# Kernel tuning notes

Hardware: AMD Instinct MI355X
Metric: run time of the kernel (lower is better)

Reference implementation:

```python
import jax, jax.numpy as jnp
import numpy as np

B, S, IN, HID, H, D, FF = 8, 2048, 512, 512, 8, 64, 2048
EPS = 1e-5


def layer_norm(x, g, b):
    m = jnp.mean(x, axis=-1, keepdims=True)
    v = jnp.mean(jnp.square(x - m), axis=-1, keepdims=True)
    return (x - m) * jax.lax.rsqrt(v + EPS) * g + b


def delta_rule(q, k, v, beta):
    # q,k,v: [S,B,H,D]; beta: [S,B,H,1]
    # W_t = W_{t-1} + beta_t*(v_t - W_{t-1} k_t) k_t^T ; out_t = W_t q_t
    def step(W, inp):
        qt, kt, vt, bt = inp
        wk = jnp.einsum('bhde,bhe->bhd', W, kt)
        v_new = bt * (vt - wk)
        W = W + jnp.einsum('bhd,bhe->bhde', v_new, kt)
        out = jnp.einsum('bhde,bhe->bhd', W, qt)
        return W, out

    bsz = q.shape[1]
    W0 = jnp.zeros((bsz, H, D, D), dtype=q.dtype)
    _, outs = jax.lax.scan(step, W0, (q, k, v, beta))
    return outs  # [S,B,H,D]


def fast_ff(x, ln_g, ln_b, slow_w, out_w):
    # x: [S,B,HID]
    slen, bsz, _ = x.shape
    h = layer_norm(x, ln_g, ln_b)
    qkvb = jnp.einsum('sbi,oi->sbo', h, slow_w).reshape(slen, bsz, H, 3 * D + 1)
    q, k, v, beta = jnp.split(qkvb, [D, 2 * D, 3 * D], axis=-1)
    q = jax.nn.softmax(q, axis=-1)
    k = jax.nn.softmax(k, axis=-1)
    beta = jax.nn.sigmoid(beta)
    attn = delta_rule(q, k, v, beta)  # [S,B,H,D]
    o = jnp.einsum('sbd,od->sbo', attn.reshape(slen, bsz, H * D), out_w)
    return x + o


def ffn(x, ln_g, ln_b, w1, b1, w2, b2):
    h = layer_norm(x, ln_g, ln_b)
    h = jax.nn.relu(jnp.einsum('sbi,fi->sbf', h, w1) + b1)
    return x + jnp.einsum('sbf,of->sbo', h, w2) + b2


def setup_inputs() -> dict:
    key = jax.random.key(0)
    ks = jax.random.split(key, 8)
    s = 0.02
    return {
        'x': jax.random.normal(ks[0], (B, S, IN), jnp.float32),
        'ip_w': s * jax.random.normal(ks[1], (HID, IN), jnp.float32),
        'ip_b': jnp.zeros((HID,), jnp.float32),
        'fw_ln_g': jnp.ones((2, HID), jnp.float32),
        'fw_ln_b': jnp.zeros((2, HID), jnp.float32),
        'fw_slow_w': s * jax.random.normal(ks[2], (2, H * (3 * D + 1), HID), jnp.float32),
        'fw_out_w': s * jax.random.normal(ks[3], (2, HID, H * D), jnp.float32),
        'ff_ln_g': jnp.ones((HID,), jnp.float32),
        'ff_ln_b': jnp.zeros((HID,), jnp.float32),
        'ff_w1': s * jax.random.normal(ks[4], (FF, HID), jnp.float32),
        'ff_b1': jnp.zeros((FF,), jnp.float32),
        'ff_w2': s * jax.random.normal(ks[5], (HID, FF), jnp.float32),
        'ff_b2': jnp.zeros((HID,), jnp.float32),
    }


def reference(x, ip_w, ip_b, fw_ln_g, fw_ln_b, fw_slow_w, fw_out_w,
              ff_ln_g, ff_ln_b, ff_w1, ff_b1, ff_w2, ff_b2):
    out = jnp.einsum('bsi,hi->bsh', x, ip_w) + ip_b  # input_proj
    out = out.transpose(1, 0, 2)  # [S,B,HID]
    out = fast_ff(out, fw_ln_g[0], fw_ln_b[0], fw_slow_w[0], fw_out_w[0])
    out = ffn(out, ff_ln_g, ff_ln_b, ff_w1, ff_b1, ff_w2, ff_b2)
    out = fast_ff(out, fw_ln_g[1], fw_ln_b[1], fw_slow_w[1], fw_out_w[1])
    return out.transpose(1, 0, 2)  # [B,S,HID]
```

## Files before the change

### kernel.cpp

```cpp
#include <hip/hip_runtime.h>
#include <hip/hip_bf16.h>

#define B_    8
#define S_    2048
#define HID_  512
#define H_    8
#define D_    64
#define FF_   2048
#define QN_   1664
#define NCH_  32
#define SLOWSTRIDE (1544 * 512)

typedef unsigned short u16;
typedef __attribute__((ext_vector_type(8))) short short8;
typedef __attribute__((ext_vector_type(4))) float f32x4;

__device__ __forceinline__ u16 f2bf(float x) {
  unsigned u = __builtin_bit_cast(unsigned, x);
  unsigned r = (u + 0x7FFFu + ((u >> 16) & 1u)) >> 16;
  return (u16)r;
}
__device__ __forceinline__ float bf2f(u16 v) {
  return __builtin_bit_cast(float, (unsigned)v << 16);
}
__device__ __forceinline__ void gload16(const void* g, void* l) {
  __builtin_amdgcn_global_load_lds(
      (const __attribute__((address_space(1))) unsigned int*)g,
      (__attribute__((address_space(3))) unsigned int*)l, 16, 0, 0);
}

template<int FS, int GS>
__device__ __forceinline__ void prod64(const u16* __restrict__ F,
                                       const u16* __restrict__ G,
                                       int wrow0, int lane, f32x4 acc[4])
{
  short8 f0 = *(const short8*)&F[(wrow0 + (lane & 15)) * FS + ((lane >> 4) * 8)];
  short8 f1 = *(const short8*)&F[(wrow0 + (lane & 15)) * FS + 32 + ((lane >> 4) * 8)];
  #pragma unroll
  for (int c0 = 0; c0 < 4; ++c0) {
    short8 g0 = *(const short8*)&G[(c0 * 16 + (lane & 15)) * GS + ((lane >> 4) * 8)];
    short8 g1 = *(const short8*)&G[(c0 * 16 + (lane & 15)) * GS + 32 + ((lane >> 4) * 8)];
    acc[c0] = __builtin_amdgcn_mfma_f32_16x16x32_bf16(f0, g0, acc[c0], 0, 0, 0);
    acc[c0] = __builtin_amdgcn_mfma_f32_16x16x32_bf16(f1, g1, acc[c0], 0, 0, 0);
  }
}

template<bool BIAS, bool RELU, bool RES, bool OUTBF, bool TRANS, bool QKVB>
__global__ __launch_bounds__(256, 4) void gemm_bf(
    const u16* __restrict__ A, const u16* __restrict__ W,
    const float* __restrict__ bias, const float* __restrict__ res,
    void* __restrict__ Cout, int M, int N, int K, int nx)
{
  __shared__ __align__(16) u16 SH[16384];
  const int tid = threadIdx.x, lane = tid & 63, wv = tid >> 6;
  const int nwg = gridDim.x;
  const int l = ((blockIdx.x & 7) * (nwg >> 3)) + (blockIdx.x >> 3);
  const int bm = (l / nx) * 128, bn = (l % nx) * 128;
  const int wr = wv >> 1, wc = wv & 1;
  const int row16 = lane & 15, kg = lane >> 4;
  const int srow = lane >> 2;
  const int ssoff = ((lane & 3) ^ (srow & 3)) * 16;

  f32x4 acc[4][4] = {};
  const int ktiles = K >> 5;

  auto STAGE = [&](int buf, int kt) {
    u16* As = &SH[buf * 8192];
    u16* Bs = &SH[buf * 8192 + 4096];
    #pragma unroll
    for (int i = 0; i < 2; ++i) {
      const int r = i * 64 + wv * 16;
      const char* ga = (const char*)(A + (size_t)(bm + r + srow) * K + (size_t)kt * 32) + ssoff;
      gload16(ga, &As[r * 32]);
      const char* gw = (const char*)(W + (size_t)(bn + r + srow) * K + (size_t)kt * 32) + ssoff;
      gload16(gw, &Bs[r * 32]);
    }
  };

  STAGE(0, 0);
  __syncthreads();
  int buf = 0;
  for (int kt = 0; kt < ktiles; ++kt) {
    if (kt + 1 < ktiles) STAGE(buf ^ 1, kt + 1);
    const u16* As = &SH[buf * 8192];
    const u16* Bs = &SH[buf * 8192 + 4096];
    short8 af[4], bf_[4];
    #pragma unroll
    for (int m = 0; m < 4; ++m) {
      const int lrow = wr * 64 + m * 16 + row16;
      af[m] = *(const short8*)&As[lrow * 32 + (kg ^ (lrow & 3)) * 8];
    }
    #pragma unroll
    for (int n = 0; n < 4; ++n) {
      const int lrow = wc * 64 + n * 16 + row16;
      bf_[n] = *(const short8*)&Bs[lrow * 32 + (kg ^ (lrow & 3)) * 8];
    }
    #pragma unroll
    for (int m = 0; m < 4; ++m)
      #pragma unroll
      for (int n = 0; n < 4; ++n)
        acc[m][n] = __builtin_amdgcn_mfma_f32_16x16x32_bf16(af[m], bf_[n], acc[m][n], 0, 0, 0);
    __syncthreads();
    buf ^= 1;
  }

  if (QKVB) {
    const int span0 = bn + wc * 64;
    #pragma unroll
    for (int m = 0; m < 4; ++m) {
      #pragma unroll
      for (int j = 0; j < 4; ++j) {
        if (span0 < 1024) {
          float v0 = acc[m][0][j], v1 = acc[m][1][j];
          float v2 = acc[m][2][j], v3 = acc[m][3][j];
          float mx = fmaxf(fmaxf(v0, v1), fmaxf(v2, v3));
          #pragma unroll
          for (int off = 1; off < 16; off <<= 1) mx = fmaxf(mx, __shfl_xor(mx, off));
          float e0 = __expf(v0 - mx), e1 = __expf(v1 - mx);
          float e2 = __expf(v2 - mx), e3 = __expf(v3 - mx);
          float s = (e0 + e1) + (e2 + e3);
          #pragma unroll
          for (int off = 1; off < 16; off <<= 1) s += __shfl_xor(s, off);
          float r = 1.f / s;
          acc[m][0][j] = e0 * r; acc[m][1][j] = e1 * r;
          acc[m][2][j] = e2 * r; acc[m][3][j] = e3 * r;
        } else if (span0 >= 1536) {
          #pragma unroll
          for (int n = 0; n < 4; ++n)
            acc[m][n][j] = 1.f / (1.f + __expf(-acc[m][n][j]));
        }
      }
    }
  }

  float* LD = (float*)SH;
  #pragma unroll
  for (int p = 0; p < 4; ++p) {
    if (p) __syncthreads();
    if (wr == (p >> 1)) {
      #pragma unroll
      for (int mm = 0; mm < 2; ++mm) {
        const int m = (p & 1) * 2 + mm;
        #pragma unroll
        for (int n = 0; n < 4; ++n)
          #pragma unroll
          for (int j = 0; j < 4; ++j)
            LD[(mm * 16 + kg * 4 + j) * 132 + wc * 64 + n * 16 + row16] = acc[m][n][j];
      }
    }
    __syncthreads();
    #pragma unroll
    for (int step = 0; step < 4; ++step) {
      int linear = step * 256 + tid;
      int row = linear >> 5, q = linear & 31;
      float4 v = *(const float4*)&LD[row * 132 + q * 4];
      const int grow = bm + p * 32 + row;
      const int gcol = bn + q * 4;
      if (BIAS) {
        float4 b4 = *(const float4*)&bias[gcol];
        v.x += b4.x; v.y += b4.y; v.z += b4.z; v.w += b4.w;
      }
      if (RES) {
        float4 r4 = *(const float4*)&res[(size_t)grow * N + gcol];
        v.x += r4.x; v.y += r4.y; v.z += r4.z; v.w += r4.w;
      }
      if (RELU) {
        v.x = fmaxf(v.x, 0.f); v.y = fmaxf(v.y, 0.f);
        v.z = fmaxf(v.z, 0.f); v.w = fmaxf(v.w, 0.f);
      }
      size_t gr = TRANS ? ((size_t)(grow & 7) * S_ + (grow >> 3)) : (size_t)grow;
      if (OUTBF) {
        uint2 pk;
        pk.x = (unsigned)f2bf(v.x) | ((unsigned)f2bf(v.y) << 16);
        pk.y = (unsigned)f2bf(v.z) | ((unsigned)f2bf(v.w) << 16);
        *(uint2*)&((u16*)Cout)[gr * N + gcol] = pk;
      } else {
        *(float4*)&((float*)Cout)[gr * N + gcol] = v;
      }
    }
  }
}

__global__ __launch_bounds__(256) void conv_w(const float* __restrict__ s,
                                              u16* __restrict__ d, int n, int npad)
{
  int i = blockIdx.x * 256 + threadIdx.x;
  if (i < npad) d[i] = (i < n) ? f2bf(s[i]) : (u16)0;
}

__global__ __launch_bounds__(256) void conv_slow(const float* __restrict__ s,
                                                 u16* __restrict__ d)
{
  int r = blockIdx.x;
  int src;
  if (r < 512)       src = (r >> 6) * 193 + (r & 63);
  else if (r < 1024) src = ((r - 512) >> 6) * 193 + 64 + (r & 63);
  else if (r < 1536) src = ((r - 1024) >> 6) * 193 + 128 + (r & 63);
  else if (r < 1544) src = (r - 1536) * 193 + 192;
  else               src = -1;
  for (int c = threadIdx.x; c < 512; c += 256)
    d[(size_t)r * 512 + c] = (src >= 0) ? f2bf(s[(size_t)src * 512 + c]) : (u16)0;
}

__global__ __launch_bounds__(64) void conv_x(const float* __restrict__ x,
                                             u16* __restrict__ xbf)
{
  size_t m = blockIdx.x;
  size_t s = m >> 3, b = m & 7;
  const float4* src = (const float4*)(x + (b * (size_t)S_ + s) * HID_);
  float4 v0 = src[threadIdx.x], v1 = src[64 + threadIdx.x];
  u16* dst = xbf + m * HID_;
  uint2 p0, p1;
  p0.x = (unsigned)f2bf(v0.x) | ((unsigned)f2bf(v0.y) << 16);
  p0.y = (unsigned)f2bf(v0.z) | ((unsigned)f2bf(v0.w) << 16);
  p1.x = (unsigned)f2bf(v1.x) | ((unsigned)f2bf(v1.y) << 16);
  p1.y = (unsigned)f2bf(v1.z) | ((unsigned)f2bf(v1.w) << 16);
  *(uint2*)&dst[threadIdx.x * 4] = p0;
  *(uint2*)&dst[256 + threadIdx.x * 4] = p1;
}

__global__ __launch_bounds__(64) void ln_bf(const float* __restrict__ x,
    const float* __restrict__ g, const float* __restrict__ bt,
    u16* __restrict__ o)
{
  size_t row = blockIdx.x;
  int lane = threadIdx.x;
  const float4* xr = (const float4*)(x + row * HID_);
  float4 v0 = xr[lane];
  float4 v1 = xr[64 + lane];
  float s  = v0.x + v0.y + v0.z + v0.w + v1.x + v1.y + v1.z + v1.w;
  float ss = v0.x*v0.x + v0.y*v0.y + v0.z*v0.z + v0.w*v0.w
           + v1.x*v1.x + v1.y*v1.y + v1.z*v1.z + v1.w*v1.w;
  #pragma unroll
  for (int off = 32; off; off >>= 1) {
    s  += __shfl_xor(s, off);
    ss += __shfl_xor(ss, off);
  }
  float mean = s * (1.f / HID_);
  float inv  = rsqrtf(ss * (1.f / HID_) - mean * mean + 1e-5f);
  const float4* gv = (const float4*)g;
  const float4* bv = (const float4*)bt;
  float4 g0 = gv[lane], g1 = gv[64 + lane];
  float4 b0 = bv[lane], b1 = bv[64 + lane];
  uint2 p0, p1;
  p0.x = (unsigned)f2bf((v0.x - mean) * inv * g0.x + b0.x)
       | ((unsigned)f2bf((v0.y - mean) * inv * g0.y + b0.y) << 16);
  p0.y = (unsigned)f2bf((v0.z - mean) * inv * g0.z + b0.z)
       | ((unsigned)f2bf((v0.w - mean) * inv * g0.w + b0.w) << 16);
  p1.x = (unsigned)f2bf((v1.x - mean) * inv * g1.x + b1.x)
       | ((unsigned)f2bf((v1.y - mean) * inv * g1.y + b1.y) << 16);
  p1.y = (unsigned)f2bf((v1.z - mean) * inv * g1.z + b1.z)
       | ((unsigned)f2bf((v1.w - mean) * inv * g1.w + b1.w) << 16);
  u16* ov = o + row * HID_;
  *(uint2*)&ov[lane * 4] = p0;
  *(uint2*)&ov[256 + lane * 4] = p1;
}

__global__ __launch_bounds__(256, 3) void delta_p1(const u16* __restrict__ qf,
                                                   u16* __restrict__ MTg,
                                                   u16* __restrict__ Ng,
                                                   u16* __restrict__ CKg,
                                                   u16* __restrict__ U0Tg)
{
  __shared__ __align__(16) u16 Kb[64 * 72];
  __shared__ __align__(16) u16 AmKT[64 * 72];
  __shared__ __align__(16) u16 stV[16 * 72];
  __shared__ __align__(16) u16 stK[16 * 72];
  __shared__ __align__(16) u16 CKTb[64 * 72];
  __shared__ __align__(16) u16 U0Tb[64 * 72];
  __shared__ float bet[64];

  const int id5 = blockIdx.x, bh = id5 >> 5;
  const int b = bh & 7, h = bh >> 3, t0 = (id5 & 31) * 64;
  const int tid = threadIdx.x, lane = tid & 63, wv = tid >> 6;
  const int wid = wv, wrow0 = wv * 16;
  const size_t mb = (size_t)id5 * 4096;

  #pragma unroll
  for (int p = 0; p < 2; ++p) {
    int linear = p * 256 + tid, row = linear >> 3, seg = linear & 7;
    uint4 k4 = *(const uint4*)&qf[((size_t)(t0 + row) * B_ + b) * QN_ + 512 + h * 64 + seg * 8];
    *(short8*)&Kb[row * 72 + seg * 8] = __builtin_bit_cast(short8, k4);
  }
  if (tid < 64) bet[tid] = bf2f(qf[((size_t)(t0 + tid) * B_ + b) * QN_ + 1536 + h]);
  __syncthreads();

  {
    f32x4 a[4] = {};
    prod64<72, 72>(Kb, Kb, wrow0, lane, a);
    #pragma unroll
    for (int c0 = 0; c0 < 4; ++c0)
      #pragma unroll
      for (int j = 0; j < 4; ++j) {
        int row = wrow0 + (lane >> 4) * 4 + j, col = c0 * 16 + (lane & 15);
        AmKT[col * 72 + row] = f2bf(bet[row] * a[c0][j]);
      }
  }

  float uv[16], uk[16];
  #pragma unroll
  for (int i = 0; i < 16; ++i) {
    const int row = wrow0 + i;
    const float bt_ = bet[row];
    uv[i] = bt_ * bf2f(qf[((size_t)(t0 + row) * B_ + b) * QN_ + 1024 + h * 64 + lane]);
    uk[i] = bt_ * bf2f(Kb[row * 72 + lane]);
  }
  __syncthreads();

  #pragma unroll 1
  for (int blk = 0; blk < 4; ++blk) {
    if (wid == blk) {
      const int r0 = blk * 16;
      #pragma unroll
      for (int jj = 0; jj < 15; ++jj) {
        short8 a0 = *(const short8*)&AmKT[(r0 + jj) * 72 + r0];
        short8 a1 = *(const short8*)&AmKT[(r0 + jj) * 72 + r0 + 8];
        float uvj = uv[jj], ukj = uk[jj];
        #pragma unroll
        for (int t = jj + 1; t < 16; ++t) {
          float a = bf2f((u16)(t < 8 ? a0[t] : a1[t - 8]));
          uv[t] = fmaf(-a, uvj, uv[t]);
          uk[t] = fmaf(-a, ukj, uk[t]);
        }
      }
      {
        union { u16 u[16]; short8 s[2]; } pv, pk;
        #pragma unroll
        for (int i = 0; i < 16; ++i) { pv.u[i] = f2bf(uv[i]); pk.u[i] = f2bf(uk[i]); }
        *(short8*)&stV[lane * 18 + 0] = pv.s[0];
        *(short8*)&stV[lane * 18 + 8] = pv.s[1];
        *(short8*)&stK[lane * 18 + 0] = pk.s[0];
        *(short8*)&stK[lane * 18 + 8] = pk.s[1];
      }
    }
    __syncthreads();
    if (wid > blk) {
      const int r0 = blk * 16;
      #pragma unroll
      for (int jj = 0; jj < 16; ++jj) {
        short8 a0 = *(const short8*)&AmKT[(r0 + jj) * 72 + wrow0];
        short8 a1 = *(const short8*)&AmKT[(r0 + jj) * 72 + wrow0 + 8];
        float sv = bf2f(stV[lane * 18 + jj]);
        float sk = bf2f(stK[lane * 18 + jj]);
        #pragma unroll
        for (int i = 0; i < 16; ++i) {
          float a = bf2f((u16)(i < 8 ? a0[i] : a1[i - 8]));
          uv[i] = fmaf(-a, sv, uv[i]);
          uk[i] = fmaf(-a, sk, uk[i]);
        }
      }
    }
    __syncthreads();
  }

  {
    union { u16 u[16]; short8 s[2]; } pk, pu;
    #pragma unroll
    for (int i = 0; i < 16; ++i) { pk.u[i] = f2bf(uk[i]); pu.u[i] = f2bf(uv[i]); }
    *(short8*)&CKTb[lane * 72 + wrow0]     = pk.s[0];
    *(short8*)&CKTb[lane * 72 + wrow0 + 8] = pk.s[1];
    *(short8*)&U0Tb[lane * 72 + wrow0]     = pu.s[0];
    *(short8*)&U0Tb[lane * 72 + wrow0 + 8] = pu.s[1];
  }
  const int prow = tid >> 2, pc0 = (tid & 3) * 16;
  {
    union { u16 u[16]; short8 s[2]; } pt;
    #pragma unroll
    for (int i = 0; i < 16; ++i) pt.u[i] = Kb[(pc0 + i) * 72 + prow];
    *(short8*)&AmKT[prow * 72 + pc0]     = pt.s[0];
    *(short8*)&AmKT[prow * 72 + pc0 + 8] = pt.s[1];
  }
  __syncthreads();

  {
    f32x4 am[4] = {}, an[4] = {};
    prod64<72, 72>(AmKT, CKTb, wrow0, lane, am);
    prod64<72, 72>(U0Tb, AmKT, wrow0, lane, an);
    #pragma unroll
    for (int c0 = 0; c0 < 4; ++c0)
      #pragma unroll
      for (int j = 0; j < 4; ++j) {
        int row = wrow0 + (lane >> 4) * 4 + j, col = c0 * 16 + (lane & 15);
        MTg[mb + (size_t)row * 64 + col] = f2bf(am[c0][j]);
        Ng[mb + (size_t)row * 64 + col]  = f2bf(an[c0][j]);
      }
    union { u16 u[16]; uint4 v[2]; } pc;
    #pragma unroll
    for (int i = 0; i < 16; ++i) pc.u[i] = CKTb[(pc0 + i) * 72 + prow];
    *(uint4*)&CKg[mb + prow * 64 + pc0]     = pc.v[0];
    *(uint4*)&CKg[mb + prow * 64 + pc0 + 8] = pc.v[1];
    short8 a0 = *(const short8*)&U0Tb[prow * 72 + pc0];
    short8 a1 = *(const short8*)&U0Tb[prow * 72 + pc0 + 8];
    *(uint4*)&U0Tg[mb + prow * 64 + pc0]     = __builtin_bit_cast(uint4, a0);
    *(uint4*)&U0Tg[mb + prow * 64 + pc0 + 8] = __builtin_bit_cast(uint4, a1);
  }
}

__global__ __launch_bounds__(256, 1) void delta_p2(const u16* __restrict__ MTg,
                                                   const u16* __restrict__ Ng,
                                                   u16* __restrict__ Wsnap)
{
  __shared__ float Ws[64][65];
  __shared__ __align__(16) u16 Wbf[64 * 72];
  __shared__ __align__(16) u16 MTb[64 * 72];
  __shared__ __align__(16) u16 Nb[64 * 72];
  const int bh = blockIdx.x;
  const int tid = threadIdx.x, lane = tid & 63, wv = tid >> 6, wrow0 = wv * 16;
  const int prow = tid >> 2, pc0 = (tid & 3) * 16;

  for (int i = tid; i < 64 * 65; i += 256) (&Ws[0][0])[i] = 0.f;
  for (int i = tid; i < 64 * 72; i += 256) Wbf[i] = 0;
  __syncthreads();

  size_t base = (size_t)bh * NCH_ * 4096;
  uint4 rm0 = *(const uint4*)&MTg[base + prow * 64 + pc0];
  uint4 rm1 = *(const uint4*)&MTg[base + prow * 64 + pc0 + 8];
  uint4 rn0 = *(const uint4*)&Ng[base + prow * 64 + pc0];
  uint4 rn1 = *(const uint4*)&Ng[base + prow * 64 + pc0 + 8];

  for (int j = 0; j < NCH_; ++j) {
    *(short8*)&MTb[prow * 72 + pc0]     = __builtin_bit_cast(short8, rm0);
    *(short8*)&MTb[prow * 72 + pc0 + 8] = __builtin_bit_cast(short8, rm1);
    *(short8*)&Nb[prow * 72 + pc0]      = __builtin_bit_cast(short8, rn0);
    *(short8*)&Nb[prow * 72 + pc0 + 8]  = __builtin_bit_cast(short8, rn1);
    {
      size_t sb = base + (size_t)j * 4096;
      short8 w0 = *(const short8*)&Wbf[prow * 72 + pc0];
      short8 w1 = *(const short8*)&Wbf[prow * 72 + pc0 + 8];
      *(uint4*)&Wsnap[sb + prow * 64 + pc0]     = __builtin_bit_cast(uint4, w0);
      *(uint4*)&Wsnap[sb + prow * 64 + pc0 + 8] = __builtin_bit_cast(uint4, w1);
    }
    if (j + 1 < NCH_) {
      size_t nb2 = base + (size_t)(j + 1) * 4096;
      rm0 = *(const uint4*)&MTg[nb2 + prow * 64 + pc0];
      rm1 = *(const uint4*)&MTg[nb2 + prow * 64 + pc0 + 8];
      rn0 = *(const uint4*)&Ng[nb2 + prow * 64 + pc0];
      rn1 = *(const uint4*)&Ng[nb2 + prow * 64 + pc0 + 8];
    }
    __syncthreads();
    f32x4 a[4] = {};
    prod64<72, 72>(Wbf, MTb, wrow0, lane, a);
    #pragma unroll
    for (int c0 = 0; c0 < 4; ++c0)
      #pragma unroll
      for (int jj = 0; jj < 4; ++jj) {
        int row = wrow0 + (lane >> 4) * 4 + jj, col = c0 * 16 + (lane & 15);
        float w = Ws[row][col] + bf2f(Nb[row * 72 + col]) - a[c0][jj];
        Ws[row][col] = w;
        Wbf[row * 72 + col] = f2bf(w);
      }
    __syncthreads();
  }
}

__global__ __launch_bounds__(256, 2) void delta_p3(const u16* __restrict__ qf,
                                                   const u16* __restrict__ Wsnap,
                                                   const u16* __restrict__ CKg,
                                                   const u16* __restrict__ U0Tg,
                                                   u16* __restrict__ attnb)
{
  __shared__ __align__(16) u16 Qb[64 * 72];
  __shared__ __align__(16) u16 Kb[64 * 72];
  __shared__ __align__(16) u16 W0b[64 * 72];
  __shared__ __align__(16) u16 CKb[64 * 72];
  __shared__ __align__(16) u16 U0Tb[64 * 72];
  __shared__ __align__(16) u16 Gb[64 * 72];
  __shared__ __align__(16) u16 UTb[64 * 72];

  const int id5 = blockIdx.x, bh = id5 >> 5;
  const int b = bh & 7, h = bh >> 3, t0 = (id5 & 31) * 64;
  const int tid = threadIdx.x, lane = tid & 63, wv = tid >> 6, wrow0 = wv * 16;
  const int prow = tid >> 2, pc0 = (tid & 3) * 16;
  const size_t mb = (size_t)id5 * 4096;

  #pragma unroll
  for (int p = 0; p < 2; ++p) {
    int linear = p * 256 + tid, row = linear >> 3, seg = linear & 7;
    size_t gb = ((size_t)(t0 + row) * B_ + b) * QN_;
    uint4 q4 = *(const uint4*)&qf[gb + h * 64 + seg * 8];
    uint4 k4 = *(const uint4*)&qf[gb + 512 + h * 64 + seg * 8];
    uint4 w4 = *(const uint4*)&Wsnap[mb + (size_t)row * 64 + seg * 8];
    *(short8*)&Qb[row * 72 + seg * 8]  = __builtin_bit_cast(short8, q4);
    *(short8*)&Kb[row * 72 + seg * 8]  = __builtin_bit_cast(short8, k4);
    *(short8*)&W0b[row * 72 + seg * 8] = __builtin_bit_cast(short8, w4);
  }
  {
    uint4 c0v = *(const uint4*)&CKg[mb + prow * 64 + pc0];
    uint4 c1v = *(const uint4*)&CKg[mb + prow * 64 + pc0 + 8];
    uint4 u0v = *(const uint4*)&U0Tg[mb + prow * 64 + pc0];
    uint4 u1v = *(const uint4*)&U0Tg[mb + prow * 64 + pc0 + 8];
    *(short8*)&CKb[prow * 72 + pc0]      = __builtin_bit_cast(short8, c0v);
    *(short8*)&CKb[prow * 72 + pc0 + 8]  = __builtin_bit_cast(short8, c1v);
    *(short8*)&U0Tb[prow * 72 + pc0]     = __builtin_bit_cast(short8, u0v);
    *(short8*)&U0Tb[prow * 72 + pc0 + 8] = __builtin_bit_cast(short8, u1v);
  }
  __syncthreads();

  f32x4 ag[4] = {}, ac[4] = {}, ab[4] = {};
  prod64<72, 72>(Qb, Kb, wrow0, lane, ag);
  prod64<72, 72>(W0b, CKb, wrow0, lane, ac);
  prod64<72, 72>(Qb, W0b, wrow0, lane, ab);

  #pragma unroll
  for (int c0 = 0; c0 < 4; ++c0)
    #pragma unroll
    for (int j = 0; j < 4; ++j) {
      int row = wrow0 + (lane >> 4) * 4 + j, col = c0 * 16 + (lane & 15);
      Gb[row * 72 + col]  = f2bf(col <= row ? ag[c0][j] : 0.f);
      UTb[row * 72 + col] = f2bf(bf2f(U0Tb[row * 72 + col]) - ac[c0][j]);
    }
  __syncthreads();

  prod64<72, 72>(Gb, UTb, wrow0, lane, ab);

  #pragma unroll
  for (int c0 = 0; c0 < 4; ++c0)
    #pragma unroll
    for (int j = 0; j < 4; ++j) {
      int row = wrow0 + (lane >> 4) * 4 + j, col = c0 * 16 + (lane & 15);
      attnb[((size_t)(t0 + row) * B_ + b) * HID_ + h * 64 + col] = f2bf(ab[c0][j]);
    }
}

extern "C" void kernel_launch(void* const* d_in, const int* in_sizes, int n_in,
                              void* d_out, int out_size, void* d_ws, size_t ws_size,
                              hipStream_t stream)
{
  const float* x        = (const float*)d_in[0];
  const float* ip_w     = (const float*)d_in[1];
  const float* ip_b     = (const float*)d_in[2];
  const float* fw_ln_g  = (const float*)d_in[3];
  const float* fw_ln_b  = (const float*)d_in[4];
  const float* fw_slow_w = (const float*)d_in[5];
  const float* fw_out_w  = (const float*)d_in[6];
  const float* ff_ln_g  = (const float*)d_in[7];
  const float* ff_ln_b  = (const float*)d_in[8];
  const float* ff_w1    = (const float*)d_in[9];
  const float* ff_b1    = (const float*)d_in[10];
  const float* ff_w2    = (const float*)d_in[11];
  const float* ff_b2    = (const float*)d_in[12];
  float* out = (float*)d_out;

  const int M = B_ * S_;
  const size_t matN = (size_t)64 * NCH_ * 4096;

  const size_t nIp = 512 * 512, nOut = 512 * 512;
  const size_t nSlow = (size_t)QN_ * 512;
  const size_t nW1 = (size_t)FF_ * 512, nW2 = (size_t)512 * FF_;
  const size_t nXbf = (size_t)M * HID_;
  const size_t poolElems = nIp + 2 * nSlow + 2 * nOut + nW1 + nW2 + nXbf + matN;

  size_t need = (size_t)M * HID_ * 4
              + ((size_t)M * QN_ + 2 * matN + poolElems) * 2;
  if (ws_size < need) return;

  float* cur   = (float*)d_ws;
  u16*   qkvbf = (u16*)(cur + (size_t)M * HID_);
  u16*   attnSlot = qkvbf + (size_t)M * QN_;
  u16*   MTg   = attnSlot;
  u16*   Ng    = MTg + matN;
  u16*   attnb = attnSlot;
  u16*   CKg   = (u16*)out;
  u16*   U0Tg  = CKg + matN;
  u16*   tmpbf = (u16*)out;
  u16*   hiddenb = qkvbf;

  u16* pool = attnSlot + 2 * matN;
  u16* ipwb   = pool;               pool += nIp;
  u16* slowb0 = pool;               pool += nSlow;
  u16* slowb1 = pool;               pool += nSlow;
  u16* outwb0 = pool;               pool += nOut;
  u16* outwb1 = pool;               pool += nOut;
  u16* w1b    = pool;               pool += nW1;
  u16* w2b    = pool;               pool += nW2;
  u16* Wsnap  = pool;               pool += matN;
  u16* xbf    = pool;

  dim3 blk(256);

  conv_w<<<(nIp + 255) / 256, blk, 0, stream>>>(ip_w, ipwb, nIp, nIp);
  conv_slow<<<QN_, blk, 0, stream>>>(fw_slow_w, slowb0);
  conv_slow<<<QN_, blk, 0, stream>>>(fw_slow_w + (size_t)SLOWSTRIDE, slowb1);
  conv_w<<<(nOut + 255) / 256, blk, 0, stream>>>(fw_out_w, outwb0, nOut, nOut);
  conv_w<<<(nOut + 255) / 256, blk, 0, stream>>>(fw_out_w + (size_t)512 * 512, outwb1, nOut, nOut);
  conv_w<<<(nW1 + 255) / 256, blk, 0, stream>>>(ff_w1, w1b, nW1, nW1);
  conv_w<<<(nW2 + 255) / 256, blk, 0, stream>>>(ff_w2, w2b, nW2, nW2);
  conv_x<<<M, 64, 0, stream>>>(x, xbf);

  gemm_bf<true, false, false, false, false, false><<<4 * 128, blk, 0, stream>>>(
      xbf, ipwb, ip_b, nullptr, cur, M, HID_, HID_, 4);

  for (int layer = 0; layer < 2; ++layer) {
    u16* slowb = layer ? slowb1 : slowb0;
    u16* outwb = layer ? outwb1 : outwb0;

    ln_bf<<<M, 64, 0, stream>>>(cur, fw_ln_g + layer * HID_, fw_ln_b + layer * HID_, tmpbf);
    gemm_bf<false, false, false, true, false, true><<<13 * 128, blk, 0, stream>>>(
        tmpbf, slowb, nullptr, nullptr, qkvbf, M, QN_, HID_, 13);
    delta_p1<<<64 * NCH_, 256, 0, stream>>>(qkvbf, MTg, Ng, CKg, U0Tg);
    delta_p2<<<64, 256, 0, stream>>>(MTg, Ng, Wsnap);
    delta_p3<<<64 * NCH_, 256, 0, stream>>>(qkvbf, Wsnap, CKg, U0Tg, attnb);
    if (layer == 0) {
      gemm_bf<false, false, true, false, false, false><<<4 * 128, blk, 0, stream>>>(
          attnb, outwb, nullptr, cur, cur, M, HID_, HID_, 4);
      ln_bf<<<M, 64, 0, stream>>>(cur, ff_ln_g, ff_ln_b, tmpbf);
      gemm_bf<true, true, false, true, false, false><<<16 * 128, blk, 0, stream>>>(
          tmpbf, w1b, ff_b1, nullptr, hiddenb, M, FF_, HID_, 16);
      gemm_bf<true, false, true, false, false, false><<<4 * 128, blk, 0, stream>>>(
          hiddenb, w2b, ff_b2, cur, cur, M, HID_, FF_, 4);
    } else {
      gemm_bf<false, false, true, false, true, false><<<4 * 128, blk, 0, stream>>>(
          attnb, outwb, nullptr, cur, out, M, HID_, HID_, 4);
    }
  }
}
```

Baseline: 521.8 us.

## Split delta state recurrence across row groups and fuse weight conversions

The sequential chunk-state kernel is split so each block owns 16 rows of the 64x64 state. This gives 256 blocks instead of 64 and shortens per-step MFMA work, at the cost of each block redundantly loading the full MT chunk. The seven weight-conversion launches are merged into one kernel, cutting launch overhead. The output kernel reuses the Q/K shared buffers for G/UT, which needs an extra barrier, to lower LDS use and allow three blocks per CU.

```diff
diff --git a/kernel.cpp b/kernel.cpp
--- a/kernel.cpp
+++ b/kernel.cpp
@@ -181,25 +181,54 @@
   }
 }
 
-__global__ __launch_bounds__(256) void conv_w(const float* __restrict__ s,
-                                              u16* __restrict__ d, int n, int npad)
-{
-  int i = blockIdx.x * 256 + threadIdx.x;
-  if (i < npad) d[i] = (i < n) ? f2bf(s[i]) : (u16)0;
-}
-
-__global__ __launch_bounds__(256) void conv_slow(const float* __restrict__ s,
-                                                 u16* __restrict__ d)
-{
-  int r = blockIdx.x;
-  int src;
-  if (r < 512)       src = (r >> 6) * 193 + (r & 63);
-  else if (r < 1024) src = ((r - 512) >> 6) * 193 + 64 + (r & 63);
-  else if (r < 1536) src = ((r - 1024) >> 6) * 193 + 128 + (r & 63);
-  else if (r < 1544) src = (r - 1536) * 193 + 192;
-  else               src = -1;
-  for (int c = threadIdx.x; c < 512; c += 256)
-    d[(size_t)r * 512 + c] = (src >= 0) ? f2bf(s[(size_t)src * 512 + c]) : (u16)0;
+__global__ __launch_bounds__(256) void conv_all(
+    const float* __restrict__ ip_w, const float* __restrict__ slow_w,
+    const float* __restrict__ out_w, const float* __restrict__ w1,
+    const float* __restrict__ w2,
+    u16* __restrict__ ipwb, u16* __restrict__ slowb0, u16* __restrict__ slowb1,
+    u16* __restrict__ outwb0, u16* __restrict__ outwb1,
+    u16* __restrict__ w1b, u16* __restrict__ w2b)
+{
+  int bid = blockIdx.x;
+  const int tid = threadIdx.x;
+  if (bid < 1024) {
+    int i = bid * 256 + tid;
+    ipwb[i] = f2bf(ip_w[i]);
+    return;
+  }
+  bid -= 1024;
+  if (bid < 2 * QN_) {
+    int layer = bid / QN_, r = bid % QN_;
+    const float* s = slow_w + (size_t)layer * SLOWSTRIDE;
+    u16* d = (layer ? slowb1 : slowb0);
+    int src;
+    if (r < 512)       src = (r >> 6) * 193 + (r & 63);
+    else if (r < 1024) src = ((r - 512) >> 6) * 193 + 64 + (r & 63);
+    else if (r < 1536) src = ((r - 1024) >> 6) * 193 + 128 + (r & 63);
+    else if (r < 1544) src = (r - 1536) * 193 + 192;
+    else               src = -1;
+    for (int c = tid; c < 512; c += 256)
+      d[(size_t)r * 512 + c] = (src >= 0) ? f2bf(s[(size_t)src * 512 + c]) : (u16)0;
+    return;
+  }
+  bid -= 2 * QN_;
+  if (bid < 2048) {
+    int layer = bid >> 10;
+    int i = (bid & 1023) * 256 + tid;
+    (layer ? outwb1 : outwb0)[i] = f2bf(out_w[(size_t)layer * 262144 + i]);
+    return;
+  }
+  bid -= 2048;
+  if (bid < 4096) {
+    int i = bid * 256 + tid;
+    w1b[i] = f2bf(w1[i]);
+    return;
+  }
+  bid -= 4096;
+  {
+    int i = bid * 256 + tid;
+    w2b[i] = f2bf(w2[i]);
+  }
 }
 
 __global__ __launch_bounds__(64) void conv_x(const float* __restrict__ x,
@@ -396,64 +425,66 @@
   }
 }
 
-__global__ __launch_bounds__(256, 1) void delta_p2(const u16* __restrict__ MTg,
+__global__ __launch_bounds__(256, 2) void delta_p2(const u16* __restrict__ MTg,
                                                    const u16* __restrict__ Ng,
                                                    u16* __restrict__ Wsnap)
 {
-  __shared__ float Ws[64][65];
-  __shared__ __align__(16) u16 Wbf[64 * 72];
   __shared__ __align__(16) u16 MTb[64 * 72];
-  __shared__ __align__(16) u16 Nb[64 * 72];
-  const int bh = blockIdx.x;
-  const int tid = threadIdx.x, lane = tid & 63, wv = tid >> 6, wrow0 = wv * 16;
+  __shared__ __align__(16) u16 Nb[16 * 72];
+  __shared__ __align__(16) u16 Wbf[16 * 72];
+  __shared__ float Ws[16][68];
+  const int blk = blockIdx.x, bh = blk >> 2, rg = blk & 3;
+  const int tid = threadIdx.x, lane = tid & 63, wv = tid >> 6;
+  const int r0 = rg * 16;
   const int prow = tid >> 2, pc0 = (tid & 3) * 16;
-
-  for (int i = tid; i < 64 * 65; i += 256) (&Ws[0][0])[i] = 0.f;
-  for (int i = tid; i < 64 * 72; i += 256) Wbf[i] = 0;
+  const int nrow = tid >> 4, nc0 = (tid & 15) * 4;
+
+  for (int i = tid; i < 16 * 72; i += 256) Wbf[i] = 0;
+  for (int i = tid; i < 16 * 68; i += 256) (&Ws[0][0])[i] = 0.f;
   __syncthreads();
 
   size_t base = (size_t)bh * NCH_ * 4096;
   uint4 rm0 = *(const uint4*)&MTg[base + prow * 64 + pc0];
   uint4 rm1 = *(const uint4*)&MTg[base + prow * 64 + pc0 + 8];
-  uint4 rn0 = *(const uint4*)&Ng[base + prow * 64 + pc0];
-  uint4 rn1 = *(const uint4*)&Ng[base + prow * 64 + pc0 + 8];
+  uint2 rn  = *(const uint2*)&Ng[base + (size_t)(r0 + nrow) * 64 + nc0];
 
   for (int j = 0; j < NCH_; ++j) {
     *(short8*)&MTb[prow * 72 + pc0]     = __builtin_bit_cast(short8, rm0);
     *(short8*)&MTb[prow * 72 + pc0 + 8] = __builtin_bit_cast(short8, rm1);
-    *(short8*)&Nb[prow * 72 + pc0]      = __builtin_bit_cast(short8, rn0);
-    *(short8*)&Nb[prow * 72 + pc0 + 8]  = __builtin_bit_cast(short8, rn1);
+    *(uint2*)&Nb[nrow * 72 + nc0] = rn;
     {
       size_t sb = base + (size_t)j * 4096;
-      short8 w0 = *(const short8*)&Wbf[prow * 72 + pc0];
-      short8 w1 = *(const short8*)&Wbf[prow * 72 + pc0 + 8];
-      *(uint4*)&Wsnap[sb + prow * 64 + pc0]     = __builtin_bit_cast(uint4, w0);
-      *(uint4*)&Wsnap[sb + prow * 64 + pc0 + 8] = __builtin_bit_cast(uint4, w1);
+      uint2 w2v = *(const uint2*)&Wbf[nrow * 72 + nc0];
+      *(uint2*)&Wsnap[sb + (size_t)(r0 + nrow) * 64 + nc0] = w2v;
     }
     if (j + 1 < NCH_) {
       size_t nb2 = base + (size_t)(j + 1) * 4096;
       rm0 = *(const uint4*)&MTg[nb2 + prow * 64 + pc0];
       rm1 = *(const uint4*)&MTg[nb2 + prow * 64 + pc0 + 8];
-      rn0 = *(const uint4*)&Ng[nb2 + prow * 64 + pc0];
-      rn1 = *(const uint4*)&Ng[nb2 + prow * 64 + pc0 + 8];
+      rn  = *(const uint2*)&Ng[nb2 + (size_t)(r0 + nrow) * 64 + nc0];
     }
     __syncthreads();
-    f32x4 a[4] = {};
-    prod64<72, 72>(Wbf, MTb, wrow0, lane, a);
-    #pragma unroll
-    for (int c0 = 0; c0 < 4; ++c0)
-      #pragma unroll
-      for (int jj = 0; jj < 4; ++jj) {
-        int row = wrow0 + (lane >> 4) * 4 + jj, col = c0 * 16 + (lane & 15);
-        float w = Ws[row][col] + bf2f(Nb[row * 72 + col]) - a[c0][jj];
-        Ws[row][col] = w;
-        Wbf[row * 72 + col] = f2bf(w);
-      }
+    f32x4 acc = {};
+    {
+      short8 f0 = *(const short8*)&Wbf[(lane & 15) * 72 + (lane >> 4) * 8];
+      short8 f1 = *(const short8*)&Wbf[(lane & 15) * 72 + 32 + (lane >> 4) * 8];
+      short8 g0 = *(const short8*)&MTb[(wv * 16 + (lane & 15)) * 72 + (lane >> 4) * 8];
+      short8 g1 = *(const short8*)&MTb[(wv * 16 + (lane & 15)) * 72 + 32 + (lane >> 4) * 8];
+      acc = __builtin_amdgcn_mfma_f32_16x16x32_bf16(f0, g0, acc, 0, 0, 0);
+      acc = __builtin_amdgcn_mfma_f32_16x16x32_bf16(f1, g1, acc, 0, 0, 0);
+    }
+    #pragma unroll
+    for (int jj = 0; jj < 4; ++jj) {
+      int row = (lane >> 4) * 4 + jj, col = wv * 16 + (lane & 15);
+      float w = Ws[row][col] + bf2f(Nb[row * 72 + col]) - acc[jj];
+      Ws[row][col] = w;
+      Wbf[row * 72 + col] = f2bf(w);
+    }
     __syncthreads();
   }
 }
 
-__global__ __launch_bounds__(256, 2) void delta_p3(const u16* __restrict__ qf,
+__global__ __launch_bounds__(256, 3) void delta_p3(const u16* __restrict__ qf,
                                                    const u16* __restrict__ Wsnap,
                                                    const u16* __restrict__ CKg,
                                                    const u16* __restrict__ U0Tg,
@@ -464,8 +495,8 @@
   __shared__ __align__(16) u16 W0b[64 * 72];
   __shared__ __align__(16) u16 CKb[64 * 72];
   __shared__ __align__(16) u16 U0Tb[64 * 72];
-  __shared__ __align__(16) u16 Gb[64 * 72];
-  __shared__ __align__(16) u16 UTb[64 * 72];
+  u16* Gb  = Qb;
+  u16* UTb = Kb;
 
   const int id5 = blockIdx.x, bh = id5 >> 5;
   const int b = bh & 7, h = bh >> 3, t0 = (id5 & 31) * 64;
@@ -500,6 +531,7 @@
   prod64<72, 72>(Qb, Kb, wrow0, lane, ag);
   prod64<72, 72>(W0b, CKb, wrow0, lane, ac);
   prod64<72, 72>(Qb, W0b, wrow0, lane, ab);
+  __syncthreads();
 
   #pragma unroll
   for (int c0 = 0; c0 < 4; ++c0)
@@ -578,13 +610,8 @@
 
   dim3 blk(256);
 
-  conv_w<<<(nIp + 255) / 256, blk, 0, stream>>>(ip_w, ipwb, nIp, nIp);
-  conv_slow<<<QN_, blk, 0, stream>>>(fw_slow_w, slowb0);
-  conv_slow<<<QN_, blk, 0, stream>>>(fw_slow_w + (size_t)SLOWSTRIDE, slowb1);
-  conv_w<<<(nOut + 255) / 256, blk, 0, stream>>>(fw_out_w, outwb0, nOut, nOut);
-  conv_w<<<(nOut + 255) / 256, blk, 0, stream>>>(fw_out_w + (size_t)512 * 512, outwb1, nOut, nOut);
-  conv_w<<<(nW1 + 255) / 256, blk, 0, stream>>>(ff_w1, w1b, nW1, nW1);
-  conv_w<<<(nW2 + 255) / 256, blk, 0, stream>>>(ff_w2, w2b, nW2, nW2);
+  conv_all<<<14592, blk, 0, stream>>>(ip_w, fw_slow_w, fw_out_w, ff_w1, ff_w2,
+                                      ipwb, slowb0, slowb1, outwb0, outwb1, w1b, w2b);
   conv_x<<<M, 64, 0, stream>>>(x, xbf);
 
   gemm_bf<true, false, false, false, false, false><<<4 * 128, blk, 0, stream>>>(
@@ -598,7 +625,7 @@
     gemm_bf<false, false, false, true, false, true><<<13 * 128, blk, 0, stream>>>(
         tmpbf, slowb, nullptr, nullptr, qkvbf, M, QN_, HID_, 13);
     delta_p1<<<64 * NCH_, 256, 0, stream>>>(qkvbf, MTg, Ng, CKg, U0Tg);
-    delta_p2<<<64, 256, 0, stream>>>(MTg, Ng, Wsnap);
+    delta_p2<<<256, 256, 0, stream>>>(MTg, Ng, Wsnap);
     delta_p3<<<64 * NCH_, 256, 0, stream>>>(qkvbf, Wsnap, CKg, U0Tg, attnb);
     if (layer == 0) {
       gemm_bf<false, false, true, false, false, false><<<4 * 128, blk, 0, stream>>>(
```

After: 473.0 us, median of 2. 9.3% less time.
